# Performance work log

Measured on AMD Instinct MI355X. Metric: run time of the kernel, lower is better.

Reference implementation:

```python
import jax, jax.numpy as jnp
import numpy as np

B, S, D = 1, 2048, 4096
NH, NKV, HD = 32, 8, 128          # n_heads, n_kv_heads, head_dim
N_REP = NH // NKV                  # repeat_kv factor (GQA)
ROPE_THETA = 10000.0


def setup_inputs() -> dict:
    key = jax.random.key(0)
    ks = jax.random.split(key, 5)
    x = jax.random.normal(ks[0], (B, S, D), jnp.float32)
    wq = jax.random.normal(ks[1], (D, NH * HD), jnp.float32) * (1.0 / np.sqrt(D))
    wk = jax.random.normal(ks[2], (D, NKV * HD), jnp.float32) * (1.0 / np.sqrt(D))
    wv = jax.random.normal(ks[3], (D, NKV * HD), jnp.float32) * (1.0 / np.sqrt(D))
    wo = jax.random.normal(ks[4], (NH * HD, D), jnp.float32) * (1.0 / np.sqrt(NH * HD))
    # freqs_cis = exp(i * t * theta^{-2j/hd}); store as cos/sin, shape (S, HD//2)
    inv_freq = 1.0 / (ROPE_THETA ** (np.arange(0, HD, 2, dtype=np.float32) / HD))
    angles = np.outer(np.arange(S, dtype=np.float32), inv_freq)
    return {"x": x, "wq": wq, "wk": wk, "wv": wv, "wo": wo,
            "cos": jnp.asarray(np.cos(angles), jnp.float32),
            "sin": jnp.asarray(np.sin(angles), jnp.float32)}


def _rope(t, cos, sin):
    # t: (b, s, h, hd); pairs (t[...,2j], t[...,2j+1]) form complex numbers
    tr, ti = t[..., 0::2], t[..., 1::2]
    c = cos[None, :, None, :]
    s = sin[None, :, None, :]
    out = jnp.stack([tr * c - ti * s, tr * s + ti * c], axis=-1)  # re-interleave
    return out.reshape(t.shape)


def reference(x, wq, wk, wv, wo, cos, sin):
    b, s, _ = x.shape
    q = (x @ wq).reshape(b, s, NH, HD)
    k = (x @ wk).reshape(b, s, NKV, HD)
    v = (x @ wv).reshape(b, s, NKV, HD)
    q = _rope(q, cos, sin)
    k = _rope(k, cos, sin)
    # prefill with start_pos=0: KV cache slice == fresh k, v
    # repeat_kv == torch.repeat_interleave along head dim
    k = jnp.repeat(k, N_REP, axis=2)  # (b, s, NH, HD)
    v = jnp.repeat(v, N_REP, axis=2)
    q = q.transpose(0, 2, 1, 3)  # (b, NH, s, hd)
    k = k.transpose(0, 2, 1, 3)
    v = v.transpose(0, 2, 1, 3)
    scores = jnp.einsum('bhqd,bhkd->bhqk', q, k) / jnp.sqrt(jnp.float32(HD))
    causal = jnp.tril(jnp.ones((s, s), bool))
    scores = jnp.where(causal[None, None], scores, jnp.float32(-1e30))
    probs = jax.nn.softmax(scores, axis=-1)
    out = jnp.einsum('bhqk,bhkd->bhqd', probs, v)
    out = out.transpose(0, 2, 1, 3).reshape(b, s, NH * HD)
    return out @ wo
```

## Files before the change

kernel.cpp:

```cpp
#include <hip/hip_runtime.h>
#include <stdint.h>

typedef unsigned short ushort_t;
typedef short bf16x4 __attribute__((ext_vector_type(4)));
typedef short bf16x8 __attribute__((ext_vector_type(8)));
typedef float f32x4 __attribute__((ext_vector_type(4)));
typedef float f32x16 __attribute__((ext_vector_type(16)));
typedef float f32x4v __attribute__((ext_vector_type(4)));

__device__ __forceinline__ ushort_t f2bf(float f) {
  unsigned int u = __builtin_bit_cast(unsigned int, f);
  u += 0x7fffu + ((u >> 16) & 1u);
  return (ushort_t)(u >> 16);
}
__device__ __forceinline__ float bf2f(ushort_t h) {
  unsigned int u = ((unsigned int)h) << 16;
  return __builtin_bit_cast(float, u);
}
__device__ __forceinline__ float exp2_hw(float x) {
  return __builtin_amdgcn_exp2f(x);
}
__device__ __forceinline__ void load_lds16(const void* g, void* l) {
  __builtin_amdgcn_global_load_lds(
      (const __attribute__((address_space(1))) void*)g,
      (__attribute__((address_space(3))) void*)l, 16, 0, 0);
}

__global__ __launch_bounds__(256) void cvt_x_kernel(const float* __restrict__ x,
                                                    ushort_t* __restrict__ xb) {
  int i = blockIdx.x * 256 + threadIdx.x;
  const f32x4v* xv = (const f32x4v*)x;
  f32x4v a = xv[2 * i], b = xv[2 * i + 1];
  bf16x8 o;
  o[0] = (short)f2bf(a[0]); o[1] = (short)f2bf(a[1]);
  o[2] = (short)f2bf(a[2]); o[3] = (short)f2bf(a[3]);
  o[4] = (short)f2bf(b[0]); o[5] = (short)f2bf(b[1]);
  o[6] = (short)f2bf(b[2]); o[7] = (short)f2bf(b[3]);
  ((bf16x8*)xb)[i] = o;
}

__global__ __launch_bounds__(256) void tr_cvt_kernel(const float* __restrict__ src,
                                                     ushort_t* __restrict__ dst,
                                                     int R, int C) {
  __shared__ float tile[64][65];
  int r0 = blockIdx.y * 64, c0 = blockIdx.x * 64;
  int t = threadIdx.x;
#pragma unroll
  for (int i = 0; i < 4; i++) {
    int idx = t + i * 256;
    int r = idx >> 4, c4 = idx & 15;
    f32x4v v = *(const f32x4v*)&src[(size_t)(r0 + r) * C + c0 + c4 * 4];
#pragma unroll
    for (int j = 0; j < 4; j++) tile[r][c4 * 4 + j] = v[j];
  }
  __syncthreads();
#pragma unroll
  for (int i = 0; i < 4; i++) {
    int idx = t + i * 256;
    int cr = idx >> 4, cg = idx & 15;
    bf16x4 o;
#pragma unroll
    for (int j = 0; j < 4; j++) o[j] = (short)f2bf(tile[cg * 4 + j][cr]);
    *(bf16x4*)&dst[(size_t)(c0 + cr) * R + r0 + cg * 4] = o;
  }
}

__global__ __launch_bounds__(256) void rope_kernel(ushort_t* __restrict__ C1,
                                                   const float* __restrict__ cosb,
                                                   const float* __restrict__ sinb) {
  int idx = blockIdx.x * 256 + threadIdx.x;
  int s = idx / 640;
  int col0 = (idx % 640) * 8;
  int i0 = (col0 & 127) >> 1;
  const float qs = (col0 < 4096) ? 0.12753055296570565f : 1.0f;
  ushort_t* p = C1 + (size_t)s * 6144 + col0;
  bf16x8 v = *(const bf16x8*)p;
  bf16x8 o;
  const float* cr = cosb + s * 64 + i0;
  const float* sr = sinb + s * 64 + i0;
#pragma unroll
  for (int j = 0; j < 4; j++) {
    float tr = bf2f((ushort_t)v[2 * j]);
    float ti = bf2f((ushort_t)v[2 * j + 1]);
    float c = cr[j], sn = sr[j];
    o[2 * j] = (short)f2bf((tr * c - ti * sn) * qs);
    o[2 * j + 1] = (short)f2bf((tr * sn + ti * c) * qs);
  }
  *(bf16x8*)p = o;
}

__global__ __launch_bounds__(256) void trv_kernel(const ushort_t* __restrict__ C1,
                                                  ushort_t* __restrict__ VT) {
  __shared__ ushort_t tile[64][65];
  int c0 = blockIdx.x * 64;
  int r0 = blockIdx.y * 64;
  int t = threadIdx.x;
#pragma unroll
  for (int i = 0; i < 16; i++) {
    int idx = t + i * 256;
    int r = idx >> 6, c = idx & 63;
    tile[r][c] = C1[(size_t)(r0 + r) * 6144 + 5120 + c0 + c];
  }
  __syncthreads();
#pragma unroll
  for (int i = 0; i < 16; i++) {
    int idx = t + i * 256;
    int cr = idx >> 6, cc = idx & 63;
    VT[(size_t)(c0 + cr) * 2048 + r0 + cc] = tile[cc][cr];
  }
}

__device__ __forceinline__ void xcd_chunk_map(int id, int nby, int nbx,
                                              int& browi, int& bcoli) {
  const int xcd = id & 7;
  const int j = id >> 3;
  const int rch = nby >> 1, cch = nbx >> 2;
  const int cr = xcd >> 2, cc = xcd & 3;
  const int r = j / cch, c = j % cch;
  browi = cr * rch + r;
  bcoli = cc * cch + c;
}

template <typename OutT>
__global__ __launch_bounds__(512) void gemmC_kernel(const ushort_t* __restrict__ A,
                                                    const ushort_t* __restrict__ BT,
                                                    OutT* __restrict__ C,
                                                    int M, int N, int K, int ldc) {
  __shared__ ushort_t As[2][256 * 64];
  __shared__ ushort_t Bs[3][192 * 64];
  const int nbx = N / 192, nby = M >> 8;
  int browi, bcoli;
  xcd_chunk_map((int)blockIdx.x, nby, nbx, browi, bcoli);
  const int brow = browi << 8, bcol = bcoli * 192;
  const int tid = threadIdx.x, w = tid >> 6, lane = tid & 63;
  const int wr = w >> 2, wc = w & 3;
  const int lr = lane & 15, lk = lane >> 4;

  const ushort_t* Ab = A + (size_t)brow * K;
  const ushort_t* Bb = BT + (size_t)bcol * K;

  auto stageQ = [&](const ushort_t* gbase, char* lds, int t, int q) {
    int L = q * 512 + tid;
    int r = L >> 3, sc = L & 7;
    load_lds16(gbase + (size_t)r * K + (t << 6) + ((sc ^ (r & 7)) << 3), lds + L * 16);
  };

  f32x4 acc[8][3] = {};
  const int NT = K >> 6;

#pragma unroll
  for (int q = 0; q < 3; ++q) stageQ(Bb, (char*)&Bs[0][0], 0, q);
  stageQ(Ab, (char*)&As[0][0], 0, 0);
  stageQ(Ab, (char*)&As[0][0], 0, 2);
  stageQ(Ab, (char*)&As[0][0], 0, 1);
  stageQ(Ab, (char*)&As[0][0], 0, 3);
#pragma unroll
  for (int q = 0; q < 3; ++q) stageQ(Bb, (char*)&Bs[1][0], 1, q);
  asm volatile("s_waitcnt vmcnt(3)" ::: "memory");
  __builtin_amdgcn_s_barrier();

  int bcur = 0;
  for (int t = 0; t < NT; ++t) {
    const int c = t & 1;
    const char* Ac = (const char*)&As[c][0];
    const char* Bc = (const char*)&Bs[bcur][0];
    char* An = (char*)&As[c ^ 1][0];
    const int bnxt = (bcur + 2 >= 3) ? bcur - 1 : bcur + 2;
    char* Bn = (char*)&Bs[bnxt][0];
    const bool pfA = (t + 1 < NT), pfB = (t + 2 < NT);

    bf16x8 af[4][2], bfr[3][2];
#pragma unroll
    for (int mm = 0; mm < 4; ++mm)
#pragma unroll
      for (int ks = 0; ks < 2; ++ks) {
        int rA = wr * 128 + mm * 16 + lr;
        af[mm][ks] = *(const bf16x8*)(Ac + rA * 128 + (((ks * 4 + lk) ^ (rA & 7)) << 4));
      }
#pragma unroll
    for (int n = 0; n < 3; ++n)
#pragma unroll
      for (int ks = 0; ks < 2; ++ks) {
        int rB = wc * 48 + n * 16 + lr;
        bfr[n][ks] = *(const bf16x8*)(Bc + rB * 128 + (((ks * 4 + lk) ^ (rB & 7)) << 4));
      }
    if (pfA) { stageQ(Ab, An, t + 1, 0); stageQ(Ab, An, t + 1, 2); }
    if (pfB) stageQ(Bb, Bn, t + 2, 0);
    __builtin_amdgcn_s_barrier();
    asm volatile("s_waitcnt lgkmcnt(0)" ::: "memory");
    __builtin_amdgcn_sched_barrier(0);
    __builtin_amdgcn_s_setprio(1);
#pragma unroll
    for (int mm = 0; mm < 4; ++mm)
#pragma unroll
      for (int n = 0; n < 3; ++n)
#pragma unroll
        for (int ks = 0; ks < 2; ++ks)
          acc[mm][n] = __builtin_amdgcn_mfma_f32_16x16x32_bf16(af[mm][ks], bfr[n][ks],
                                                               acc[mm][n], 0, 0, 0);
    __builtin_amdgcn_s_setprio(0);
    if (pfB)
      asm volatile("s_waitcnt vmcnt(5)" ::: "memory");
    else
      asm volatile("s_waitcnt vmcnt(0)" ::: "memory");
    __builtin_amdgcn_s_barrier();

#pragma unroll
    for (int mm = 0; mm < 4; ++mm)
#pragma unroll
      for (int ks = 0; ks < 2; ++ks) {
        int rA = wr * 128 + 64 + mm * 16 + lr;
        af[mm][ks] = *(const bf16x8*)(Ac + rA * 128 + (((ks * 4 + lk) ^ (rA & 7)) << 4));
      }
    if (pfA) { stageQ(Ab, An, t + 1, 1); stageQ(Ab, An, t + 1, 3); }
    if (pfB) { stageQ(Bb, Bn, t + 2, 1); stageQ(Bb, Bn, t + 2, 2); }
    __builtin_amdgcn_s_barrier();
    asm volatile("s_waitcnt lgkmcnt(0)" ::: "memory");
    __builtin_amdgcn_sched_barrier(0);
    __builtin_amdgcn_s_setprio(1);
#pragma unroll
    for (int mm = 0; mm < 4; ++mm)
#pragma unroll
      for (int n = 0; n < 3; ++n)
#pragma unroll
        for (int ks = 0; ks < 2; ++ks)
          acc[4 + mm][n] = __builtin_amdgcn_mfma_f32_16x16x32_bf16(af[mm][ks], bfr[n][ks],
                                                                   acc[4 + mm][n], 0, 0, 0);
    __builtin_amdgcn_s_setprio(0);
    if (pfB)
      asm volatile("s_waitcnt vmcnt(5)" ::: "memory");
    else
      asm volatile("s_waitcnt vmcnt(0)" ::: "memory");
    __builtin_amdgcn_s_barrier();
    bcur = (bcur + 1 == 3) ? 0 : bcur + 1;
  }
#pragma unroll
  for (int m = 0; m < 8; ++m)
#pragma unroll
    for (int n = 0; n < 3; ++n) {
      int row = brow + wr * 128 + m * 16 + lk * 4;
      int col = bcol + wc * 48 + n * 16 + lr;
#pragma unroll
      for (int j = 0; j < 4; ++j) {
        float v = acc[m][n][j];
        if constexpr (sizeof(OutT) == 2)
          C[(size_t)(row + j) * ldc + col] = (OutT)f2bf(v);
        else
          C[(size_t)(row + j) * ldc + col] = v;
      }
    }
}

template <typename OutT>
__global__ __launch_bounds__(512) void gemmD_kernel(const ushort_t* __restrict__ A,
                                                    const ushort_t* __restrict__ BT,
                                                    OutT* __restrict__ C,
                                                    int M, int N, int K, int ldc) {
  __shared__ ushort_t As[3][256 * 64];
  __shared__ ushort_t Bs[3][128 * 64];
  const int nbx = N >> 7, nby = M >> 8;
  int browi, bcoli;
  xcd_chunk_map((int)blockIdx.x, nby, nbx, browi, bcoli);
  const int brow = browi << 8, bcol = bcoli << 7;
  const int tid = threadIdx.x, w = tid >> 6, lane = tid & 63;
  const int wr = w >> 2, wc = w & 3;
  const int lr = lane & 15, lk = lane >> 4;

  const ushort_t* Ab = A + (size_t)brow * K;
  const ushort_t* Bb = BT + (size_t)bcol * K;

  auto stageQ = [&](const ushort_t* gbase, char* lds, int t, int q) {
    int L = q * 512 + tid;
    int r = L >> 3, sc = L & 7;
    load_lds16(gbase + (size_t)r * K + (t << 6) + ((sc ^ (r & 7)) << 3), lds + L * 16);
  };
  auto stageTile = [&](int t, int buf) {
#pragma unroll
    for (int q = 0; q < 4; ++q) stageQ(Ab, (char*)&As[buf][0], t, q);
#pragma unroll
    for (int q = 0; q < 2; ++q) stageQ(Bb, (char*)&Bs[buf][0], t, q);
  };

  f32x4 acc[8][2] = {};
  const int NT = K >> 6;

  stageTile(0, 0);
  stageTile(1, 1);
  asm volatile("s_waitcnt vmcnt(6)" ::: "memory");
  __builtin_amdgcn_s_barrier();

  int cur = 0;
  for (int t = 0; t < NT; ++t) {
    const char* Ac = (const char*)&As[cur][0];
    const char* Bc = (const char*)&Bs[cur][0];
    const int nxt = (cur + 2 >= 3) ? cur - 1 : cur + 2;
    char* An = (char*)&As[nxt][0];
    char* Bn = (char*)&Bs[nxt][0];
    const bool pf = (t + 2 < NT);

    bf16x8 af[4][2], bfr[2][2];
#pragma unroll
    for (int mm = 0; mm < 4; ++mm)
#pragma unroll
      for (int ks = 0; ks < 2; ++ks) {
        int rA = wr * 128 + mm * 16 + lr;
        af[mm][ks] = *(const bf16x8*)(Ac + rA * 128 + (((ks * 4 + lk) ^ (rA & 7)) << 4));
      }
#pragma unroll
    for (int n = 0; n < 2; ++n)
#pragma unroll
      for (int ks = 0; ks < 2; ++ks) {
        int rB = wc * 32 + n * 16 + lr;
        bfr[n][ks] = *(const bf16x8*)(Bc + rB * 128 + (((ks * 4 + lk) ^ (rB & 7)) << 4));
      }
    if (pf) { stageQ(Ab, An, t + 2, 0); stageQ(Ab, An, t + 2, 2); stageQ(Bb, Bn, t + 2, 0); }
    __builtin_amdgcn_s_barrier();
    asm volatile("s_waitcnt lgkmcnt(0)" ::: "memory");
    __builtin_amdgcn_sched_barrier(0);
    __builtin_amdgcn_s_setprio(1);
#pragma unroll
    for (int mm = 0; mm < 4; ++mm)
#pragma unroll
      for (int n = 0; n < 2; ++n)
#pragma unroll
        for (int ks = 0; ks < 2; ++ks)
          acc[mm][n] = __builtin_amdgcn_mfma_f32_16x16x32_bf16(af[mm][ks], bfr[n][ks],
                                                               acc[mm][n], 0, 0, 0);
    __builtin_amdgcn_s_setprio(0);
    __builtin_amdgcn_s_barrier();

#pragma unroll
    for (int mm = 0; mm < 4; ++mm)
#pragma unroll
      for (int ks = 0; ks < 2; ++ks) {
        int rA = wr * 128 + 64 + mm * 16 + lr;
        af[mm][ks] = *(const bf16x8*)(Ac + rA * 128 + (((ks * 4 + lk) ^ (rA & 7)) << 4));
      }
    if (pf) { stageQ(Ab, An, t + 2, 1); stageQ(Ab, An, t + 2, 3); stageQ(Bb, Bn, t + 2, 1); }
    __builtin_amdgcn_s_barrier();
    asm volatile("s_waitcnt lgkmcnt(0)" ::: "memory");
    __builtin_amdgcn_sched_barrier(0);
    __builtin_amdgcn_s_setprio(1);
#pragma unroll
    for (int mm = 0; mm < 4; ++mm)
#pragma unroll
      for (int n = 0; n < 2; ++n)
#pragma unroll
        for (int ks = 0; ks < 2; ++ks)
          acc[4 + mm][n] = __builtin_amdgcn_mfma_f32_16x16x32_bf16(af[mm][ks], bfr[n][ks],
                                                                   acc[4 + mm][n], 0, 0, 0);
    __builtin_amdgcn_s_setprio(0);
    if (pf)
      asm volatile("s_waitcnt vmcnt(6)" ::: "memory");
    else if (t + 1 < NT)
      asm volatile("s_waitcnt vmcnt(0)" ::: "memory");
    __builtin_amdgcn_s_barrier();
    cur = (cur == 2) ? 0 : cur + 1;
  }
#pragma unroll
  for (int m = 0; m < 8; ++m)
#pragma unroll
    for (int n = 0; n < 2; ++n) {
      int row = brow + wr * 128 + m * 16 + lk * 4;
      int col = bcol + wc * 32 + n * 16 + lr;
#pragma unroll
      for (int j = 0; j < 4; ++j) {
        float v = acc[m][n][j];
        if constexpr (sizeof(OutT) == 2)
          C[(size_t)(row + j) * ldc + col] = (OutT)f2bf(v);
        else
          C[(size_t)(row + j) * ldc + col] = v;
      }
    }
}

template <typename OutT>
__global__ __launch_bounds__(256) void gemm128_kernel(const ushort_t* __restrict__ A,
                                                      const ushort_t* __restrict__ BT,
                                                      OutT* __restrict__ C,
                                                      int M, int N, int K, int ldc) {
  __shared__ ushort_t As[128 * 32];
  __shared__ ushort_t Bs[128 * 32];
  int brow = blockIdx.y * 128, bcol = blockIdx.x * 128;
  int tid = threadIdx.x, w = tid >> 6, lane = tid & 63;
  int wr = w >> 1, wc = w & 1;
  int lr = lane & 15, lk = lane >> 4;
  f32x4 acc[4][4] = {};

  int srow = lane >> 2;
  int scol = (lane & 3) * 8;
  const ushort_t* Ab = A + (size_t)brow * K + scol;
  const ushort_t* Bb = BT + (size_t)bcol * K + scol;

  for (int kt = 0; kt < K; kt += 32) {
#pragma unroll
    for (int i = 0; i < 2; i++) {
      int seg = w * 2 + i;
      int row = seg * 16 + srow;
      load_lds16(Ab + (size_t)row * K + kt, (char*)As + seg * 1024);
      load_lds16(Bb + (size_t)row * K + kt, (char*)Bs + seg * 1024);
    }
    __syncthreads();
    bf16x8 af[4], bfr[4];
#pragma unroll
    for (int m = 0; m < 4; m++)
      af[m] = *(const bf16x8*)&As[(wr * 64 + m * 16 + lr) * 32 + lk * 8];
#pragma unroll
    for (int n = 0; n < 4; n++)
      bfr[n] = *(const bf16x8*)&Bs[(wc * 64 + n * 16 + lr) * 32 + lk * 8];
#pragma unroll
    for (int m = 0; m < 4; m++)
#pragma unroll
      for (int n = 0; n < 4; n++)
        acc[m][n] = __builtin_amdgcn_mfma_f32_16x16x32_bf16(af[m], bfr[n], acc[m][n], 0, 0, 0);
    __syncthreads();
  }
#pragma unroll
  for (int m = 0; m < 4; m++)
#pragma unroll
    for (int n = 0; n < 4; n++) {
      int row = brow + wr * 64 + m * 16 + lk * 4;
      int col = bcol + wc * 64 + n * 16 + lr;
#pragma unroll
      for (int j = 0; j < 4; j++) {
        float v = acc[m][n][j];
        if constexpr (sizeof(OutT) == 2)
          C[(size_t)(row + j) * ldc + col] = (OutT)f2bf(v);
        else
          C[(size_t)(row + j) * ldc + col] = v;
      }
    }
}

__global__ __launch_bounds__(256) void gemmS_kernel(const ushort_t* __restrict__ C1,
                                                    ushort_t* __restrict__ P) {
  int rem = blockIdx.x, rt = 0;
  while (rem > rt) { rem -= (rt + 1); rt++; }
  const int ct = rem;
  const int h = blockIdx.y, hk = h >> 2;

  __shared__ ushort_t As[128 * 32];
  __shared__ ushort_t Bs[128 * 32];
  int tid = threadIdx.x, w = tid >> 6, lane = tid & 63;
  int wr = w >> 1, wc = w & 1;
  int lr = lane & 15, lk = lane >> 4;
  f32x4 acc[4][4] = {};
  int srow = lane >> 2;
  int scol = (lane & 3) * 8;
  const ushort_t* Ab = C1 + (size_t)(rt * 128) * 6144 + h * 128 + scol;
  const ushort_t* Bb = C1 + (size_t)(ct * 128) * 6144 + 4096 + hk * 128 + scol;

  for (int kt = 0; kt < 128; kt += 32) {
#pragma unroll
    for (int i = 0; i < 2; i++) {
      int seg = w * 2 + i;
      int row = seg * 16 + srow;
      load_lds16(Ab + (size_t)row * 6144 + kt, (char*)As + seg * 1024);
      load_lds16(Bb + (size_t)row * 6144 + kt, (char*)Bs + seg * 1024);
    }
    __syncthreads();
    bf16x8 af[4], bfr[4];
#pragma unroll
    for (int m = 0; m < 4; m++)
      af[m] = *(const bf16x8*)&As[(wr * 64 + m * 16 + lr) * 32 + lk * 8];
#pragma unroll
    for (int n = 0; n < 4; n++)
      bfr[n] = *(const bf16x8*)&Bs[(wc * 64 + n * 16 + lr) * 32 + lk * 8];
#pragma unroll
    for (int m = 0; m < 4; m++)
#pragma unroll
      for (int n = 0; n < 4; n++)
        acc[m][n] = __builtin_amdgcn_mfma_f32_16x16x32_bf16(af[m], bfr[n], acc[m][n], 0, 0, 0);
    __syncthreads();
  }
  ushort_t* Pt = P + ((size_t)h * 136 + (size_t)(rt * (rt + 1) / 2) + ct) * 16384;
  const bool diag = (rt == ct);
#pragma unroll
  for (int m = 0; m < 4; m++)
#pragma unroll
    for (int n = 0; n < 4; n++) {
      int row = wr * 64 + m * 16 + lk * 4;
      int col = wc * 64 + n * 16 + lr;
#pragma unroll
      for (int j = 0; j < 4; j++) {
        float v = exp2_hw(acc[m][n][j]);
        if (diag && col > row + j) v = 0.f;
        Pt[(row + j) * 128 + col] = f2bf(v);
      }
    }
}

__global__ __launch_bounds__(256) void gemmPV_kernel(const ushort_t* __restrict__ P,
                                                     const ushort_t* __restrict__ VT,
                                                     ushort_t* __restrict__ AO) {
  const int h = blockIdx.x, hk = h >> 2;
  const int rt = 15 - (int)blockIdx.y;

  __shared__ ushort_t As[128 * 32];
  __shared__ ushort_t Bs[128 * 32];
  int tid = threadIdx.x, w = tid >> 6, lane = tid & 63;
  int wr = w >> 1, wc = w & 1;
  int lr = lane & 15, lk = lane >> 4;
  f32x4 acc[4][4] = {};
  f32x4 sacc[4] = {};
  bf16x8 ones;
#pragma unroll
  for (int j = 0; j < 8; j++) ones[j] = (short)0x3F80;
  int srow = lane >> 2;
  int scol = (lane & 3) * 8;
  const ushort_t* Ph = P + ((size_t)h * 136 + (size_t)(rt * (rt + 1) / 2)) * 16384;
  const ushort_t* Vh = VT + (size_t)hk * 128 * 2048;

  const int nks = (rt + 1) * 4;
  for (int ks = 0; ks < nks; ks++) {
    int k0 = ks * 32;
    int ctk = k0 >> 7, kin = k0 & 127;
#pragma unroll
    for (int i = 0; i < 2; i++) {
      int seg = w * 2 + i;
      int row = seg * 16 + srow;
      load_lds16(Ph + (size_t)ctk * 16384 + (size_t)row * 128 + kin + scol,
                 (char*)As + seg * 1024);
      load_lds16(Vh + (size_t)row * 2048 + k0 + scol, (char*)Bs + seg * 1024);
    }
    __syncthreads();
    bf16x8 af[4], bfr[4];
#pragma unroll
    for (int m = 0; m < 4; m++)
      af[m] = *(const bf16x8*)&As[(wr * 64 + m * 16 + lr) * 32 + lk * 8];
#pragma unroll
    for (int n = 0; n < 4; n++)
      bfr[n] = *(const bf16x8*)&Bs[(wc * 64 + n * 16 + lr) * 32 + lk * 8];
#pragma unroll
    for (int m = 0; m < 4; m++) {
#pragma unroll
      for (int n = 0; n < 4; n++)
        acc[m][n] = __builtin_amdgcn_mfma_f32_16x16x32_bf16(af[m], bfr[n], acc[m][n], 0, 0, 0);
      sacc[m] = __builtin_amdgcn_mfma_f32_16x16x32_bf16(af[m], ones, sacc[m], 0, 0, 0);
    }
    __syncthreads();
  }
  const int q0 = rt * 128;
#pragma unroll
  for (int m = 0; m < 4; m++) {
    float invs[4];
#pragma unroll
    for (int j = 0; j < 4; j++) invs[j] = 1.0f / sacc[m][j];
#pragma unroll
    for (int n = 0; n < 4; n++) {
      int row = wr * 64 + m * 16 + lk * 4;
      int col = wc * 64 + n * 16 + lr;
#pragma unroll
      for (int j = 0; j < 4; j++) {
        float v = acc[m][n][j] * invs[j];
        AO[(size_t)(q0 + row + j) * 4096 + h * 128 + col] = f2bf(v);
      }
    }
  }
}

__global__ __launch_bounds__(256) void fattn_kernel(const ushort_t* __restrict__ C1,
                                                    const ushort_t* __restrict__ VT,
                                                    ushort_t* __restrict__ AO) {
  __shared__ ushort_t Pl[4][32][72];
  const int h = blockIdx.x, hk = h >> 2;
  const int qt = gridDim.y - 1 - blockIdx.y;
  const int tid = threadIdx.x, w = tid >> 6, lane = tid & 63;
  const int lq = lane & 31, hi = lane >> 5;
  const int qw0 = qt * 128 + w * 32;
  const int qabs = qw0 + lq;

  const ushort_t* Kb = C1 + 4096 + (size_t)hk * 128;
  const ushort_t* Vb = VT + (size_t)hk * 128 * 2048;

  bf16x8 qf[8];
  {
    const ushort_t* qrow = C1 + (size_t)qabs * 6144 + h * 128;
#pragma unroll
    for (int s = 0; s < 8; s++) qf[s] = *(const bf16x8*)(qrow + s * 16 + hi * 8);
  }
  f32x16 ot[4] = {};
  float mrow = -1e30f, ssum = 0.f;

  const int ktmax = (qw0 + 31) >> 6;
  for (int kt = 0; kt <= ktmax; kt++) {
    f32x16 sg[2] = {};
#pragma unroll
    for (int g = 0; g < 2; g++) {
      bf16x8 kfa[8];
      const ushort_t* krow = Kb + (size_t)(kt * 64 + g * 32 + lq) * 6144 + hi * 8;
#pragma unroll
      for (int s = 0; s < 8; s++) kfa[s] = *(const bf16x8*)(krow + s * 16);
#pragma unroll
      for (int s = 0; s < 8; s++)
        sg[g] = __builtin_amdgcn_mfma_f32_32x32x16_bf16(kfa[s], qf[s], sg[g], 0, 0, 0);
    }
    if (kt * 64 + 63 > qw0) {
#pragma unroll
      for (int g = 0; g < 2; g++)
#pragma unroll
        for (int r = 0; r < 16; r++) {
          int key = kt * 64 + g * 32 + (r & 3) + 8 * (r >> 2) + 4 * hi;
          if (key > qabs) sg[g][r] = -1e30f;
        }
    }
    float pm = -1e30f;
#pragma unroll
    for (int g = 0; g < 2; g++)
#pragma unroll
      for (int r = 0; r < 16; r++) pm = fmaxf(pm, sg[g][r]);
    pm = fmaxf(pm, __shfl_xor(pm, 32));
    float mnew = fmaxf(mrow, pm);
    float corr = exp2_hw(mrow - mnew);
    mrow = mnew;
    float ps = 0.f;
#pragma unroll
    for (int g = 0; g < 2; g++)
#pragma unroll
      for (int r = 0; r < 16; r++) {
        float e = exp2_hw(sg[g][r] - mnew);
        sg[g][r] = e;
        ps += e;
      }
    ps += __shfl_xor(ps, 32);
    ssum = ssum * corr + ps;
    if (!__all(corr == 1.f)) {
#pragma unroll
      for (int d = 0; d < 4; d++)
#pragma unroll
        for (int r = 0; r < 16; r++) ot[d][r] *= corr;
    }
#pragma unroll
    for (int g = 0; g < 2; g++)
#pragma unroll
      for (int rq = 0; rq < 4; rq++) {
        bf16x4 pk;
#pragma unroll
        for (int j = 0; j < 4; j++) pk[j] = (short)f2bf(sg[g][rq * 4 + j]);
        *(bf16x4*)&Pl[w][lq][g * 32 + rq * 8 + hi * 4] = pk;
      }
    asm volatile("s_waitcnt lgkmcnt(0)" ::: "memory");
    bf16x8 pf[4];
#pragma unroll
    for (int s = 0; s < 4; s++) pf[s] = *(const bf16x8*)&Pl[w][lq][s * 16 + hi * 8];
#pragma unroll
    for (int d = 0; d < 4; d++) {
      bf16x8 vfa[4];
      const ushort_t* vrow = Vb + (size_t)(d * 32 + lq) * 2048 + kt * 64 + hi * 8;
#pragma unroll
      for (int s = 0; s < 4; s++) vfa[s] = *(const bf16x8*)(vrow + s * 16);
#pragma unroll
      for (int s = 0; s < 4; s++)
        ot[d] = __builtin_amdgcn_mfma_f32_32x32x16_bf16(vfa[s], pf[s], ot[d], 0, 0, 0);
    }
  }
  const float inv = 1.0f / ssum;
  ushort_t* orow = AO + (size_t)qabs * 4096 + h * 128;
#pragma unroll
  for (int d = 0; d < 4; d++)
#pragma unroll
    for (int rq = 0; rq < 4; rq++) {
      bf16x4 ok;
#pragma unroll
      for (int j = 0; j < 4; j++) ok[j] = (short)f2bf(ot[d][rq * 4 + j] * inv);
      *(bf16x4*)(orow + d * 32 + rq * 8 + hi * 4) = ok;
    }
}

extern "C" void kernel_launch(void* const* d_in, const int* in_sizes, int n_in,
                              void* d_out, int out_size, void* d_ws, size_t ws_size,
                              hipStream_t stream) {
  (void)in_sizes; (void)n_in; (void)out_size;
  const float* x    = (const float*)d_in[0];
  const float* wq   = (const float*)d_in[1];
  const float* wk   = (const float*)d_in[2];
  const float* wv   = (const float*)d_in[3];
  const float* wo   = (const float*)d_in[4];
  const float* cosb = (const float*)d_in[5];
  const float* sinb = (const float*)d_in[6];

  char* ws = (char*)d_ws;
  const bool fast = ws_size >= (215ull << 20);

  if (fast) {
    ushort_t* C1  = (ushort_t*)(ws);
    ushort_t* VT  = (ushort_t*)(ws + ((size_t)24 << 20));
    ushort_t* woT = (ushort_t*)(ws + ((size_t)28 << 20));
    ushort_t* xb  = (ushort_t*)(ws + ((size_t)60 << 20));
    ushort_t* wT  = (ushort_t*)(ws + ((size_t)76 << 20));
    ushort_t* P   = (ushort_t*)(ws + ((size_t)60 << 20));
    ushort_t* AO  = (ushort_t*)(ws + ((size_t)196 << 20));

    cvt_x_kernel<<<4096, 256, 0, stream>>>(x, xb);
    tr_cvt_kernel<<<dim3(64, 64), 256, 0, stream>>>(wq, wT, 4096, 4096);
    tr_cvt_kernel<<<dim3(16, 64), 256, 0, stream>>>(wk, wT + (size_t)4096 * 4096, 4096, 1024);
    tr_cvt_kernel<<<dim3(16, 64), 256, 0, stream>>>(wv, wT + (size_t)5120 * 4096, 4096, 1024);
    tr_cvt_kernel<<<dim3(64, 64), 256, 0, stream>>>(wo, woT, 4096, 4096);

    gemmC_kernel<ushort_t><<<256, 512, 0, stream>>>(xb, wT, C1, 2048, 6144, 4096, 6144);
    rope_kernel<<<5120, 256, 0, stream>>>(C1, cosb, sinb);
    trv_kernel<<<dim3(16, 32), 256, 0, stream>>>(C1, VT);

    gemmS_kernel<<<dim3(136, 32), 256, 0, stream>>>(C1, P);
    gemmPV_kernel<<<dim3(32, 16), 256, 0, stream>>>(P, VT, AO);

    gemmD_kernel<float><<<256, 512, 0, stream>>>(AO, woT, (float*)d_out, 2048, 4096, 4096, 4096);
  } else {
    ushort_t* xb  = (ushort_t*)(ws);
    ushort_t* wT  = (ushort_t*)(ws + ((size_t)16 << 20));
    ushort_t* C1  = (ushort_t*)(ws + ((size_t)64 << 20));
    ushort_t* VT  = (ushort_t*)(ws + ((size_t)88 << 20));
    ushort_t* AO  = xb;
    ushort_t* woT = wT;

    cvt_x_kernel<<<4096, 256, 0, stream>>>(x, xb);
    tr_cvt_kernel<<<dim3(64, 64), 256, 0, stream>>>(wq, wT, 4096, 4096);
    tr_cvt_kernel<<<dim3(16, 64), 256, 0, stream>>>(wk, wT + (size_t)4096 * 4096, 4096, 1024);
    tr_cvt_kernel<<<dim3(16, 64), 256, 0, stream>>>(wv, wT + (size_t)5120 * 4096, 4096, 1024);
    gemm128_kernel<ushort_t><<<dim3(48, 16), 256, 0, stream>>>(xb, wT, C1, 2048, 6144, 4096, 6144);
    rope_kernel<<<5120, 256, 0, stream>>>(C1, cosb, sinb);
    trv_kernel<<<dim3(16, 32), 256, 0, stream>>>(C1, VT);
    tr_cvt_kernel<<<dim3(64, 64), 256, 0, stream>>>(wo, woT, 4096, 4096);
    fattn_kernel<<<dim3(32, 16), 256, 0, stream>>>(C1, VT, AO);
    gemm128_kernel<float><<<dim3(32, 16), 256, 0, stream>>>(AO, woT, (float*)d_out, 2048, 4096, 4096, 4096);
  }
}
```

Baseline: 346.9 us.

## Fuse QK^T exp and PV into one flash-style attention kernel

Replaces the two-kernel attention path (score GEMM writing exponentiated probabilities P to global memory, then a PV GEMM reading them back) with a single fused kernel per (head, query tile). K tiles are triple-buffered in LDS with swizzled async loads, and P stays in swizzled LDS. The grid is remapped so blocks are spread across XCDs and long and short causal rows are interleaved for balance. This removes the large global P round trip and one launch. In exchange it needs large LDS usage per block (about 128 KB) and reads V directly from global into registers each iteration.

```diff
diff --git a/kernel.cpp b/kernel.cpp
--- a/kernel.cpp
+++ b/kernel.cpp
@@ -374,6 +374,168 @@
     }
 }
 
+__global__ __launch_bounds__(512) void fattn2_kernel(const ushort_t* __restrict__ C1,
+                                                     const ushort_t* __restrict__ VT,
+                                                     ushort_t* __restrict__ AO) {
+  __shared__ ushort_t Ks[3][128 * 128];
+  __shared__ ushort_t Ps[128 * 128];
+  const int id = blockIdx.x;
+  const int xcd = id & 7, j = id >> 3;
+  const int h = xcd + 8 * (j & 3), hk = h >> 2;
+  const int jr = j >> 2;
+  const int rt = (jr & 1) ? (jr >> 1) : (15 - (jr >> 1));
+  const int q0 = rt * 128;
+  const int tid = threadIdx.x, w = tid >> 6, lane = tid & 63;
+  const int wr = w >> 2, wc = w & 3;
+  const int lr = lane & 15, lk = lane >> 4;
+
+  const char* Kg = (const char*)(C1 + 4096 + (size_t)hk * 128);
+  const ushort_t* Vb = VT + (size_t)hk * 128 * 2048;
+
+  auto stageK = [&](int ct, int buf, int q) {
+    int L = q * 512 + tid;
+    int r = L >> 4, s = L & 15;
+    int g = (s & 8) | ((s & 7) ^ (r & 7));
+    load_lds16(Kg + (size_t)(ct * 128 + r) * 12288 + g * 16,
+               (char*)&Ks[buf][0] + L * 16);
+  };
+
+  bf16x8 qf[4][4];
+#pragma unroll
+  for (int mm = 0; mm < 4; ++mm) {
+    const ushort_t* qrow = C1 + (size_t)(q0 + wr * 64 + mm * 16 + lr) * 6144 + h * 128;
+#pragma unroll
+    for (int ks = 0; ks < 4; ++ks)
+      qf[mm][ks] = *(const bf16x8*)(qrow + ks * 32 + lk * 8);
+  }
+
+  f32x4 oacc[4][2] = {};
+  f32x4 sacc[4] = {};
+  bf16x8 ones;
+#pragma unroll
+  for (int e = 0; e < 8; ++e) ones[e] = (short)0x3F80;
+
+#pragma unroll
+  for (int q = 0; q < 4; ++q) stageK(0, 0, q);
+  if (rt >= 1) {
+#pragma unroll
+    for (int q = 0; q < 4; ++q) stageK(1, 1, q);
+    asm volatile("s_waitcnt vmcnt(4)" ::: "memory");
+  } else {
+    asm volatile("s_waitcnt vmcnt(0)" ::: "memory");
+  }
+  __builtin_amdgcn_s_barrier();
+
+  int cur = 0;
+  for (int ct = 0; ct <= rt; ++ct) {
+    const char* Kc = (const char*)&Ks[cur][0];
+    const int nxt = (cur + 2 >= 3) ? cur - 1 : cur + 2;
+    const bool pf = (ct + 2 <= rt);
+
+    bf16x8 vf[2][4];
+#pragma unroll
+    for (int n = 0; n < 2; ++n) {
+      const ushort_t* vrow = Vb + (size_t)(wc * 32 + n * 16 + lr) * 2048 + ct * 128;
+#pragma unroll
+      for (int ks = 0; ks < 4; ++ks)
+        vf[n][ks] = *(const bf16x8*)(vrow + ks * 32 + lk * 8);
+    }
+    bf16x8 kf[2][4];
+#pragma unroll
+    for (int n = 0; n < 2; ++n)
+#pragma unroll
+      for (int ks = 0; ks < 4; ++ks) {
+        int row = wc * 32 + n * 16 + lr;
+        int c = ks * 4 + lk;
+        int sc = (c & 8) | ((c & 7) ^ (row & 7));
+        kf[n][ks] = *(const bf16x8*)(Kc + row * 256 + sc * 16);
+      }
+    if (pf) {
+#pragma unroll
+      for (int q = 0; q < 4; ++q) stageK(ct + 2, nxt, q);
+    }
+    asm volatile("s_waitcnt lgkmcnt(0)" ::: "memory");
+    __builtin_amdgcn_sched_barrier(0);
+    f32x4 qk[4][2] = {};
+    __builtin_amdgcn_s_setprio(1);
+#pragma unroll
+    for (int mm = 0; mm < 4; ++mm)
+#pragma unroll
+      for (int n = 0; n < 2; ++n)
+#pragma unroll
+        for (int ks = 0; ks < 4; ++ks)
+          qk[mm][n] = __builtin_amdgcn_mfma_f32_16x16x32_bf16(qf[mm][ks], kf[n][ks],
+                                                              qk[mm][n], 0, 0, 0);
+    __builtin_amdgcn_s_setprio(0);
+    const bool diag = (ct == rt);
+#pragma unroll
+    for (int mm = 0; mm < 4; ++mm)
+#pragma unroll
+      for (int n = 0; n < 2; ++n) {
+        int col = wc * 32 + n * 16 + lr;
+        int cc = col >> 3, ce = col & 7;
+#pragma unroll
+        for (int jj = 0; jj < 4; ++jj) {
+          int row = wr * 64 + mm * 16 + lk * 4 + jj;
+          float v = exp2_hw(qk[mm][n][jj]);
+          if (diag && col > row) v = 0.f;
+          int sc = (cc & 8) | ((cc & 7) ^ (row & 7));
+          *(ushort_t*)((char*)&Ps[0] + row * 256 + sc * 16 + ce * 2) = f2bf(v);
+        }
+      }
+    asm volatile("s_waitcnt lgkmcnt(0)" ::: "memory");
+    __builtin_amdgcn_s_barrier();
+    bf16x8 pa[4][4];
+#pragma unroll
+    for (int mm = 0; mm < 4; ++mm)
+#pragma unroll
+      for (int ks = 0; ks < 4; ++ks) {
+        int row = wr * 64 + mm * 16 + lr;
+        int c = ks * 4 + lk;
+        int sc = (c & 8) | ((c & 7) ^ (row & 7));
+        pa[mm][ks] = *(const bf16x8*)((const char*)&Ps[0] + row * 256 + sc * 16);
+      }
+    asm volatile("s_waitcnt lgkmcnt(0)" ::: "memory");
+    __builtin_amdgcn_sched_barrier(0);
+    __builtin_amdgcn_s_setprio(1);
+#pragma unroll
+    for (int mm = 0; mm < 4; ++mm) {
+#pragma unroll
+      for (int n = 0; n < 2; ++n)
+#pragma unroll
+        for (int ks = 0; ks < 4; ++ks)
+          oacc[mm][n] = __builtin_amdgcn_mfma_f32_16x16x32_bf16(pa[mm][ks], vf[n][ks],
+                                                                oacc[mm][n], 0, 0, 0);
+#pragma unroll
+      for (int ks = 0; ks < 4; ++ks)
+        sacc[mm] = __builtin_amdgcn_mfma_f32_16x16x32_bf16(pa[mm][ks], ones,
+                                                           sacc[mm], 0, 0, 0);
+    }
+    __builtin_amdgcn_s_setprio(0);
+    if (pf)
+      asm volatile("s_waitcnt vmcnt(4)" ::: "memory");
+    else if (ct + 1 <= rt)
+      asm volatile("s_waitcnt vmcnt(0)" ::: "memory");
+    __builtin_amdgcn_s_barrier();
+    cur = (cur + 1 == 3) ? 0 : cur + 1;
+  }
+#pragma unroll
+  for (int mm = 0; mm < 4; ++mm) {
+    float invs[4];
+#pragma unroll
+    for (int jj = 0; jj < 4; ++jj) invs[jj] = 1.0f / sacc[mm][jj];
+#pragma unroll
+    for (int n = 0; n < 2; ++n) {
+      int row = wr * 64 + mm * 16 + lk * 4;
+      int col = wc * 32 + n * 16 + lr;
+#pragma unroll
+      for (int jj = 0; jj < 4; ++jj)
+        AO[(size_t)(q0 + row + jj) * 4096 + h * 128 + col] =
+            f2bf(oacc[mm][n][jj] * invs[jj]);
+    }
+  }
+}
+
 template <typename OutT>
 __global__ __launch_bounds__(256) void gemm128_kernel(const ushort_t* __restrict__ A,
                                                       const ushort_t* __restrict__ BT,
@@ -432,133 +594,6 @@
     }
 }
 
-__global__ __launch_bounds__(256) void gemmS_kernel(const ushort_t* __restrict__ C1,
-                                                    ushort_t* __restrict__ P) {
-  int rem = blockIdx.x, rt = 0;
-  while (rem > rt) { rem -= (rt + 1); rt++; }
-  const int ct = rem;
-  const int h = blockIdx.y, hk = h >> 2;
-
-  __shared__ ushort_t As[128 * 32];
-  __shared__ ushort_t Bs[128 * 32];
-  int tid = threadIdx.x, w = tid >> 6, lane = tid & 63;
-  int wr = w >> 1, wc = w & 1;
-  int lr = lane & 15, lk = lane >> 4;
-  f32x4 acc[4][4] = {};
-  int srow = lane >> 2;
-  int scol = (lane & 3) * 8;
-  const ushort_t* Ab = C1 + (size_t)(rt * 128) * 6144 + h * 128 + scol;
-  const ushort_t* Bb = C1 + (size_t)(ct * 128) * 6144 + 4096 + hk * 128 + scol;
-
-  for (int kt = 0; kt < 128; kt += 32) {
-#pragma unroll
-    for (int i = 0; i < 2; i++) {
-      int seg = w * 2 + i;
-      int row = seg * 16 + srow;
-      load_lds16(Ab + (size_t)row * 6144 + kt, (char*)As + seg * 1024);
-      load_lds16(Bb + (size_t)row * 6144 + kt, (char*)Bs + seg * 1024);
-    }
-    __syncthreads();
-    bf16x8 af[4], bfr[4];
-#pragma unroll
-    for (int m = 0; m < 4; m++)
-      af[m] = *(const bf16x8*)&As[(wr * 64 + m * 16 + lr) * 32 + lk * 8];
-#pragma unroll
-    for (int n = 0; n < 4; n++)
-      bfr[n] = *(const bf16x8*)&Bs[(wc * 64 + n * 16 + lr) * 32 + lk * 8];
-#pragma unroll
-    for (int m = 0; m < 4; m++)
-#pragma unroll
-      for (int n = 0; n < 4; n++)
-        acc[m][n] = __builtin_amdgcn_mfma_f32_16x16x32_bf16(af[m], bfr[n], acc[m][n], 0, 0, 0);
-    __syncthreads();
-  }
-  ushort_t* Pt = P + ((size_t)h * 136 + (size_t)(rt * (rt + 1) / 2) + ct) * 16384;
-  const bool diag = (rt == ct);
-#pragma unroll
-  for (int m = 0; m < 4; m++)
-#pragma unroll
-    for (int n = 0; n < 4; n++) {
-      int row = wr * 64 + m * 16 + lk * 4;
-      int col = wc * 64 + n * 16 + lr;
-#pragma unroll
-      for (int j = 0; j < 4; j++) {
-        float v = exp2_hw(acc[m][n][j]);
-        if (diag && col > row + j) v = 0.f;
-        Pt[(row + j) * 128 + col] = f2bf(v);
-      }
-    }
-}
-
-__global__ __launch_bounds__(256) void gemmPV_kernel(const ushort_t* __restrict__ P,
-                                                     const ushort_t* __restrict__ VT,
-                                                     ushort_t* __restrict__ AO) {
-  const int h = blockIdx.x, hk = h >> 2;
-  const int rt = 15 - (int)blockIdx.y;
-
-  __shared__ ushort_t As[128 * 32];
-  __shared__ ushort_t Bs[128 * 32];
-  int tid = threadIdx.x, w = tid >> 6, lane = tid & 63;
-  int wr = w >> 1, wc = w & 1;
-  int lr = lane & 15, lk = lane >> 4;
-  f32x4 acc[4][4] = {};
-  f32x4 sacc[4] = {};
-  bf16x8 ones;
-#pragma unroll
-  for (int j = 0; j < 8; j++) ones[j] = (short)0x3F80;
-  int srow = lane >> 2;
-  int scol = (lane & 3) * 8;
-  const ushort_t* Ph = P + ((size_t)h * 136 + (size_t)(rt * (rt + 1) / 2)) * 16384;
-  const ushort_t* Vh = VT + (size_t)hk * 128 * 2048;
-
-  const int nks = (rt + 1) * 4;
-  for (int ks = 0; ks < nks; ks++) {
-    int k0 = ks * 32;
-    int ctk = k0 >> 7, kin = k0 & 127;
-#pragma unroll
-    for (int i = 0; i < 2; i++) {
-      int seg = w * 2 + i;
-      int row = seg * 16 + srow;
-      load_lds16(Ph + (size_t)ctk * 16384 + (size_t)row * 128 + kin + scol,
-                 (char*)As + seg * 1024);
-      load_lds16(Vh + (size_t)row * 2048 + k0 + scol, (char*)Bs + seg * 1024);
-    }
-    __syncthreads();
-    bf16x8 af[4], bfr[4];
-#pragma unroll
-    for (int m = 0; m < 4; m++)
-      af[m] = *(const bf16x8*)&As[(wr * 64 + m * 16 + lr) * 32 + lk * 8];
-#pragma unroll
-    for (int n = 0; n < 4; n++)
-      bfr[n] = *(const bf16x8*)&Bs[(wc * 64 + n * 16 + lr) * 32 + lk * 8];
-#pragma unroll
-    for (int m = 0; m < 4; m++) {
-#pragma unroll
-      for (int n = 0; n < 4; n++)
-        acc[m][n] = __builtin_amdgcn_mfma_f32_16x16x32_bf16(af[m], bfr[n], acc[m][n], 0, 0, 0);
-      sacc[m] = __builtin_amdgcn_mfma_f32_16x16x32_bf16(af[m], ones, sacc[m], 0, 0, 0);
-    }
-    __syncthreads();
-  }
-  const int q0 = rt * 128;
-#pragma unroll
-  for (int m = 0; m < 4; m++) {
-    float invs[4];
-#pragma unroll
-    for (int j = 0; j < 4; j++) invs[j] = 1.0f / sacc[m][j];
-#pragma unroll
-    for (int n = 0; n < 4; n++) {
-      int row = wr * 64 + m * 16 + lk * 4;
-      int col = wc * 64 + n * 16 + lr;
-#pragma unroll
-      for (int j = 0; j < 4; j++) {
-        float v = acc[m][n][j] * invs[j];
-        AO[(size_t)(q0 + row + j) * 4096 + h * 128 + col] = f2bf(v);
-      }
-    }
-  }
-}
-
 __global__ __launch_bounds__(256) void fattn_kernel(const ushort_t* __restrict__ C1,
                                                     const ushort_t* __restrict__ VT,
                                                     ushort_t* __restrict__ AO) {
@@ -688,7 +723,6 @@
     ushort_t* woT = (ushort_t*)(ws + ((size_t)28 << 20));
     ushort_t* xb  = (ushort_t*)(ws + ((size_t)60 << 20));
     ushort_t* wT  = (ushort_t*)(ws + ((size_t)76 << 20));
-    ushort_t* P   = (ushort_t*)(ws + ((size_t)60 << 20));
     ushort_t* AO  = (ushort_t*)(ws + ((size_t)196 << 20));
 
     cvt_x_kernel<<<4096, 256, 0, stream>>>(x, xb);
@@ -701,8 +735,7 @@
     rope_kernel<<<5120, 256, 0, stream>>>(C1, cosb, sinb);
     trv_kernel<<<dim3(16, 32), 256, 0, stream>>>(C1, VT);
 
-    gemmS_kernel<<<dim3(136, 32), 256, 0, stream>>>(C1, P);
-    gemmPV_kernel<<<dim3(32, 16), 256, 0, stream>>>(P, VT, AO);
+    fattn2_kernel<<<512, 512, 0, stream>>>(C1, VT, AO);
 
     gemmD_kernel<float><<<256, 512, 0, stream>>>(AO, woT, (float*)d_out, 2048, 4096, 4096, 4096);
   } else {
```

Result: no change. 348.1 us (+0.3%).

## Load full K=128 tiles into swizzled LDS once in score GEMM

Applied to the files above, without the earlier changes.

The score GEMM kernel previously looped over K in 32-wide steps, each with its own loads and two barriers. It now loads the whole 128x128 A and B tiles into LDS up front, using an XOR swizzle to avoid bank conflicts. It then reads all fragments into registers and runs the MFMAs back to back. This cuts barrier and loop overhead but raises LDS use to 64KB and register pressure (32 bf16x8 fragments), which may lower occupancy.

```diff
diff --git a/kernel.cpp b/kernel.cpp
--- a/kernel.cpp
+++ b/kernel.cpp
@@ -439,40 +439,61 @@
   const int ct = rem;
   const int h = blockIdx.y, hk = h >> 2;
 
-  __shared__ ushort_t As[128 * 32];
-  __shared__ ushort_t Bs[128 * 32];
-  int tid = threadIdx.x, w = tid >> 6, lane = tid & 63;
-  int wr = w >> 1, wc = w & 1;
-  int lr = lane & 15, lk = lane >> 4;
+  __shared__ ushort_t As_[128 * 128];
+  __shared__ ushort_t Bs_[128 * 128];
+  const int tid = threadIdx.x, w = tid >> 6, lane = tid & 63;
+  const int wr = w >> 1, wc = w & 1;
+  const int lr = lane & 15, lk = lane >> 4;
+
+  const ushort_t* Ag = C1 + (size_t)(rt * 128) * 6144 + h * 128;
+  const ushort_t* Bg = C1 + (size_t)(ct * 128) * 6144 + 4096 + hk * 128;
+
+#pragma unroll
+  for (int i = 0; i < 8; ++i) {
+    int L = i * 256 + tid;
+    int r = L >> 4, s = L & 15;
+    int g = (s & 8) | ((s & 7) ^ (r & 7));
+    load_lds16(Ag + (size_t)r * 6144 + g * 8, (char*)&As_[0] + L * 16);
+  }
+#pragma unroll
+  for (int i = 0; i < 8; ++i) {
+    int L = i * 256 + tid;
+    int r = L >> 4, s = L & 15;
+    int g = (s & 8) | ((s & 7) ^ (r & 7));
+    load_lds16(Bg + (size_t)r * 6144 + g * 8, (char*)&Bs_[0] + L * 16);
+  }
+  asm volatile("s_waitcnt vmcnt(0)" ::: "memory");
+  __builtin_amdgcn_s_barrier();
+
   f32x4 acc[4][4] = {};
-  int srow = lane >> 2;
-  int scol = (lane & 3) * 8;
-  const ushort_t* Ab = C1 + (size_t)(rt * 128) * 6144 + h * 128 + scol;
-  const ushort_t* Bb = C1 + (size_t)(ct * 128) * 6144 + 4096 + hk * 128 + scol;
-
-  for (int kt = 0; kt < 128; kt += 32) {
-#pragma unroll
-    for (int i = 0; i < 2; i++) {
-      int seg = w * 2 + i;
-      int row = seg * 16 + srow;
-      load_lds16(Ab + (size_t)row * 6144 + kt, (char*)As + seg * 1024);
-      load_lds16(Bb + (size_t)row * 6144 + kt, (char*)Bs + seg * 1024);
-    }
-    __syncthreads();
-    bf16x8 af[4], bfr[4];
-#pragma unroll
-    for (int m = 0; m < 4; m++)
-      af[m] = *(const bf16x8*)&As[(wr * 64 + m * 16 + lr) * 32 + lk * 8];
-#pragma unroll
-    for (int n = 0; n < 4; n++)
-      bfr[n] = *(const bf16x8*)&Bs[(wc * 64 + n * 16 + lr) * 32 + lk * 8];
-#pragma unroll
-    for (int m = 0; m < 4; m++)
-#pragma unroll
-      for (int n = 0; n < 4; n++)
-        acc[m][n] = __builtin_amdgcn_mfma_f32_16x16x32_bf16(af[m], bfr[n], acc[m][n], 0, 0, 0);
-    __syncthreads();
-  }
+  bf16x8 af[4][4], bfr[4][4];
+#pragma unroll
+  for (int m = 0; m < 4; ++m)
+#pragma unroll
+    for (int ks = 0; ks < 4; ++ks) {
+      int row = wr * 64 + m * 16 + lr;
+      int c = ks * 4 + lk;
+      int sc = (c & 8) | ((c & 7) ^ (row & 7));
+      af[m][ks] = *(const bf16x8*)((const char*)&As_[0] + row * 256 + sc * 16);
+    }
+#pragma unroll
+  for (int n = 0; n < 4; ++n)
+#pragma unroll
+    for (int ks = 0; ks < 4; ++ks) {
+      int row = wc * 64 + n * 16 + lr;
+      int c = ks * 4 + lk;
+      int sc = (c & 8) | ((c & 7) ^ (row & 7));
+      bfr[n][ks] = *(const bf16x8*)((const char*)&Bs_[0] + row * 256 + sc * 16);
+    }
+#pragma unroll
+  for (int m = 0; m < 4; ++m)
+#pragma unroll
+    for (int n = 0; n < 4; ++n)
+#pragma unroll
+      for (int ks = 0; ks < 4; ++ks)
+        acc[m][n] = __builtin_amdgcn_mfma_f32_16x16x32_bf16(af[m][ks], bfr[n][ks],
+                                                            acc[m][n], 0, 0, 0);
+
   ushort_t* Pt = P + ((size_t)h * 136 + (size_t)(rt * (rt + 1) / 2) + ct) * 16384;
   const bool diag = (rt == ct);
 #pragma unroll
```

New measurement: 345.0 us. No clear change (-0.6%).
